# Kernel tuning notes

Hardware: AMD Instinct MI355X
Metric: run time of the kernel (lower is better)

## Reference

```python
import jax, jax.numpy as jnp
import numpy as np

# ---- module hyperparameters ----
B, L, F = 128, 720, 128
SEG = 24            # segment_length
NSEG = L // SEG     # 30 input segments
WIN = 15            # window_size
NPRED = 96 // SEG   # 4 prediction segments
D = 128             # encode_dim
H = 512             # hidden_dim
DECAY = 0.9
C = 1.0             # curvature
EPS = 1e-6
MAXN = 1.0 - 1e-5   # max radius of Poincare ball (c=1)
SQC = 1.0           # sqrt(C)

# ---- Poincare-ball manifold ops ----
def _sqnorm(x):
    return jnp.sum(x * x, axis=-1, keepdims=True)

def _norm(x):
    return jnp.sqrt(jnp.maximum(_sqnorm(x), EPS * EPS))

def _project(x):
    n = _norm(x)
    return jnp.where(n > MAXN, x * (MAXN / n), x)

def _artanh(x):
    return jnp.arctanh(jnp.clip(x, -1.0 + 1e-7, 1.0 - 1e-7))

def mobius_add(x, y):
    xy = jnp.sum(x * y, axis=-1, keepdims=True)
    x2, y2 = _sqnorm(x), _sqnorm(y)
    num = (1.0 + 2.0 * C * xy + C * y2) * x + (1.0 - C * x2) * y
    den = 1.0 + 2.0 * C * xy + C * C * x2 * y2
    return num / jnp.maximum(den, EPS)

def expmap0(v):
    n = _norm(v)
    return _project(jnp.tanh(SQC * n) * v / (SQC * n))

def logmap0(y):
    n = _norm(y)
    return _artanh(SQC * n) * y / (SQC * n)

def expmap(x, v):
    lam = 2.0 / jnp.maximum(1.0 - C * _sqnorm(x), EPS)
    n = _norm(v)
    second = jnp.tanh(SQC * lam * n / 2.0) * v / (SQC * n)
    return _project(mobius_add(x, second))

def logmap(x, y):
    d = mobius_add(-x, y)
    n = _norm(d)
    lam = 2.0 / jnp.maximum(1.0 - C * _sqnorm(x), EPS)
    return (2.0 / (SQC * lam)) * _artanh(SQC * n) * d / n


def setup_inputs() -> dict:
    key = jax.random.key(0)
    ks = jax.random.split(key, 12)
    s = 0.05
    return {
        'trend':           0.5 * jax.random.normal(ks[0], (B, L, F), jnp.float32),
        'seasonal_coarse': 0.5 * jax.random.normal(ks[1], (B, L, F), jnp.float32),
        'seasonal_fine':   0.5 * jax.random.normal(ks[2], (B, L, F), jnp.float32),
        'residual':        0.5 * jax.random.normal(ks[3], (B, L, F), jnp.float32),
        'W_t': s * jax.random.normal(ks[4], (SEG, D), jnp.float32), 'b_t': jnp.zeros((D,), jnp.float32),
        'W_c': s * jax.random.normal(ks[5], (SEG, D), jnp.float32), 'b_c': jnp.zeros((D,), jnp.float32),
        'W_f': s * jax.random.normal(ks[6], (SEG, D), jnp.float32), 'b_f': jnp.zeros((D,), jnp.float32),
        'W_r': s * jax.random.normal(ks[7], (SEG, D), jnp.float32), 'b_r': jnp.zeros((D,), jnp.float32),
        'alpha': jnp.array([0.5], jnp.float32),
        'W1': s * jax.random.normal(ks[8], (D, H), jnp.float32), 'b1': jnp.zeros((H,), jnp.float32),
        'W2': s * jax.random.normal(ks[9], (H, SEG), jnp.float32), 'b2': jnp.zeros((SEG,), jnp.float32),
    }


def reference(trend, seasonal_coarse, seasonal_fine, residual,
              W_t, b_t, W_c, b_c, W_f, b_f, W_r, b_r,
              alpha, W1, b1, W2, b2):
    b, l, f = trend.shape

    def collapse(x):  # [B,L,F] -> [B*F, NSEG, SEG]
        return x.transpose(0, 2, 1).reshape(b * f, NSEG, SEG)

    t_s, c_s, f_s, r_s = map(collapse, (trend, seasonal_coarse, seasonal_fine, residual))

    # per-segment tangent encoding (channel-independent, shared params)
    tan = (jnp.einsum('bns,sd->bnd', t_s, W_t) + b_t
           + jnp.einsum('bns,sd->bnd', c_s, W_c) + b_c
           + jnp.einsum('bns,sd->bnd', f_s, W_f) + b_f
           + jnp.einsum('bns,sd->bnd', r_s, W_r) + b_r)
    z = expmap0(tan)                     # [BF, NSEG, D] on the ball
    z_cur = z[:, -WIN:, :]

    idx = jnp.arange(WIN - 1, dtype=jnp.float32)
    w = DECAY ** (WIN - 2 - idx)
    w = w / w.sum()

    preds, latents = [], []
    for _ in range(NPRED):
        z_last = z_cur[:, -1]
        vel = logmap(z_cur[:, :-1], z_cur[:, 1:])
        avg_v = jnp.sum(vel * w[None, :, None], axis=1)    # [BF, D]
        z_next = expmap(z_last, alpha * avg_v)             # dynamics step
        latents.append(z_next)
        # reconstruction head: logmap0 -> MLP -> segment
        t0 = logmap0(z_next)
        seg = jax.nn.relu(t0 @ W1 + b1) @ W2 + b2          # [BF, SEG]
        preds.append(seg)
        z_cur = jnp.concatenate([z_cur[:, 1:], z_next[:, None]], axis=1)

    p = jnp.stack(preds, axis=1).reshape(b * f, NPRED * SEG)
    predictions = p.reshape(b, f, NPRED * SEG).transpose(0, 2, 1)  # [B, pred_len, F]
    return predictions
```

## Files before the change

kernel.cpp:

```cpp
#include <hip/hip_runtime.h>
#include <hip/hip_bf16.h>

namespace {
constexpr int kL = 720, kF = 128;
constexpr int kWin = 15;
constexpr float kEps = 1e-6f;
constexpr float kMaxN = 1.0f - 1e-5f;
constexpr int kT0off = 360;
constexpr int ZTR = 132;
constexpr int AROW = 104;
constexpr size_t kOffT0   = 0;
constexpr size_t kOffW1   = 16777216;
constexpr size_t kOffW2   = kOffW1 + 131072;
constexpr size_t kOffBt   = kOffW2 + 32768;
constexpr size_t kOffBsum = kOffBt + 73728;
constexpr size_t kOffHid  = 17825792;
constexpr size_t kWsSplit = kOffHid + 67108864;
}

typedef float f32x4 __attribute__((ext_vector_type(4)));
typedef short s16x8 __attribute__((ext_vector_type(8)));

__device__ __forceinline__ float rcp_f(float x) { return __builtin_amdgcn_rcpf(x); }
__device__ __forceinline__ float sqrt_f(float x) { return __builtin_amdgcn_sqrtf(x); }
__device__ __forceinline__ float tanh_f(float x) {
  float t = __builtin_amdgcn_exp2f(x * -2.8853900817779268f);
  return (1.0f - t) * rcp_f(1.0f + t);
}
__device__ __forceinline__ float artanh_f(float n) {
  float nc = fminf(n, 1.0f - 1e-7f);
  return 0.34657359027997264f * __builtin_amdgcn_logf((1.0f + nc) * rcp_f(1.0f - nc));
}

extern "C" __global__ __launch_bounds__(256)
void mwhf_prep(const float* __restrict__ W1, const float* __restrict__ W2,
               const float* __restrict__ W_t, const float* __restrict__ W_c,
               const float* __restrict__ W_f, const float* __restrict__ W_r,
               const float* __restrict__ b_t, const float* __restrict__ b_c,
               const float* __restrict__ b_f, const float* __restrict__ b_r,
               __hip_bfloat16* __restrict__ W1bf, __hip_bfloat16* __restrict__ W2bf,
               __hip_bfloat16* __restrict__ BtH, __hip_bfloat16* __restrict__ BtM,
               __hip_bfloat16* __restrict__ BtL, float* __restrict__ bsum)
{
  const int b = blockIdx.x, tid = threadIdx.x;
  if (b < 64) {
    const int n0 = b * 8;
    for (int e = tid; e < 1024; e += 256) {
      int n_l = e & 7, k = e >> 3;
      W1bf[(size_t)(n0 + n_l) * 128 + k] = __float2bfloat16(W1[(size_t)k * 512 + n0 + n_l]);
    }
  } else if (b < 68) {
    const int k0 = (b - 64) * 128;
    for (int e = tid; e < 4096; e += 256) {
      int p = e >> 7, k_l = e & 127;
      float v = (p < 24) ? W2[(size_t)(k0 + k_l) * 24 + p] : 0.0f;
      W2bf[(size_t)p * 512 + k0 + k_l] = __float2bfloat16(v);
    }
  } else if (b < 72) {
    const int st = b - 68;
    const float* src = (st == 0) ? W_t : (st == 1) ? W_c : (st == 2) ? W_f : W_r;
    for (int e = tid; e < 3072; e += 256) {
      int s = e >> 7, d = e & 127;
      float x = src[e];
      __hip_bfloat16 h = __float2bfloat16(x);
      float r1 = x - __bfloat162float(h);
      __hip_bfloat16 m = __float2bfloat16(r1);
      float r2 = r1 - __bfloat162float(m);
      const int o = d * 96 + st * 24 + s;
      BtH[o] = h;
      BtM[o] = m;
      BtL[o] = __float2bfloat16(r2);
    }
  } else {
    if (tid < 128) bsum[tid] = b_t[tid] + b_c[tid] + b_f[tid] + b_r[tid];
  }
}

extern "C" __global__ __launch_bounds__(256, 3)
void mwhf_k1(const float* __restrict__ trend,
             const float* __restrict__ seas_c,
             const float* __restrict__ seas_f,
             const float* __restrict__ resid,
             const __hip_bfloat16* __restrict__ BtH,
             const __hip_bfloat16* __restrict__ BtM,
             const __hip_bfloat16* __restrict__ BtL,
             const float* __restrict__ bsum,
             const float* __restrict__ alpha,
             __hip_bfloat16* __restrict__ t0_out)
{
  __shared__ __align__(16) char smem_raw[3 * 64 * AROW * 2];
  __shared__ float z2t[64];

  float* ublk = (float*)smem_raw;
  __hip_bfloat16* Ah = (__hip_bfloat16*)smem_raw;
  __hip_bfloat16* Am = Ah + 64 * AROW;
  __hip_bfloat16* Al = Am + 64 * AROW;

  const int tid = threadIdx.x;
  const int bix = blockIdx.x;
  const int bb = (bix & 7) * 16 + (bix >> 8);
  const int f0 = ((bix >> 3) & 31) * 4;
  const int row0 = bb * 128 + f0;

  for (int e = tid; e < 192; e += 256) {
    int rr = e / 48, cc = e - rr * 48;
    int off = (rr * 16 + 15) * AROW;
    ((unsigned int*)(Ah + off))[cc] = 0u;
    ((unsigned int*)(Am + off))[cc] = 0u;
    ((unsigned int*)(Al + off))[cc] = 0u;
  }
  {
    const float* ptrs[4] = {trend, seas_c, seas_f, resid};
    for (int e = tid; e < 1440; e += 256) {
      int seg = e / 96;
      int k = e - seg * 96;
      int st = k / 24, s = k - st * 24;
      const float* p = ptrs[st];
      float4 v = *(const float4*)&p[(size_t)(bb * kL + kT0off + seg * 24 + s) * kF + f0];
      float xv[4] = {v.x, v.y, v.z, v.w};
#pragma unroll
      for (int f = 0; f < 4; ++f) {
        int m = f * 16 + seg;
        __hip_bfloat16 h = __float2bfloat16(xv[f]);
        float r1 = xv[f] - __bfloat162float(h);
        __hip_bfloat16 mm = __float2bfloat16(r1);
        float r2 = r1 - __bfloat162float(mm);
        Ah[m * AROW + k] = h;
        Am[m * AROW + k] = mm;
        Al[m * AROW + k] = __float2bfloat16(r2);
      }
    }
  }
  __syncthreads();

  const int w = tid >> 6;
  const int lane = tid & 63;
  const int l16 = lane & 15, quad = lane >> 4;

  f32x4 acc0[8];
  float scale4[4], zz4[4];
  {
    f32x4 acc1[8];
    s16x8 ah[3], am[3], al[3];
    const int abase = (w * 16 + l16) * AROW + quad * 8;
#pragma unroll
    for (int ks = 0; ks < 3; ++ks) {
      ah[ks] = *(const s16x8*)(Ah + abase + ks * 32);
      am[ks] = *(const s16x8*)(Am + abase + ks * 32);
      al[ks] = *(const s16x8*)(Al + abase + ks * 32);
    }
#pragma unroll
    for (int t = 0; t < 8; ++t) { acc0[t] = (f32x4)0.f; acc1[t] = (f32x4)0.f; }
    const __hip_bfloat16* bhp = BtH + l16 * 96 + quad * 8;
    const __hip_bfloat16* bmp = BtM + l16 * 96 + quad * 8;
    const __hip_bfloat16* blp = BtL + l16 * 96 + quad * 8;
#pragma unroll
    for (int t = 0; t < 8; ++t) {
#pragma unroll
      for (int ks = 0; ks < 3; ++ks) {
        s16x8 bh = *(const s16x8*)(bhp + t * 1536 + ks * 32);
        s16x8 bm = *(const s16x8*)(bmp + t * 1536 + ks * 32);
        s16x8 bl = *(const s16x8*)(blp + t * 1536 + ks * 32);
        acc0[t] = __builtin_amdgcn_mfma_f32_16x16x32_bf16(ah[ks], bh, acc0[t], 0, 0, 0);
        acc1[t] = __builtin_amdgcn_mfma_f32_16x16x32_bf16(am[ks], bh, acc1[t], 0, 0, 0);
        acc1[t] = __builtin_amdgcn_mfma_f32_16x16x32_bf16(ah[ks], bm, acc1[t], 0, 0, 0);
        acc1[t] = __builtin_amdgcn_mfma_f32_16x16x32_bf16(al[ks], bh, acc1[t], 0, 0, 0);
        acc1[t] = __builtin_amdgcn_mfma_f32_16x16x32_bf16(ah[ks], bl, acc1[t], 0, 0, 0);
        acc1[t] = __builtin_amdgcn_mfma_f32_16x16x32_bf16(am[ks], bm, acc1[t], 0, 0, 0);
      }
    }
    float part[4] = {0.f, 0.f, 0.f, 0.f};
#pragma unroll
    for (int t = 0; t < 8; ++t) {
      float bv = bsum[t * 16 + l16];
#pragma unroll
      for (int r = 0; r < 4; ++r) {
        float v = (acc0[t][r] + acc1[t][r]) + bv;
        acc0[t][r] = v;
        part[r] += v * v;
      }
    }
#pragma unroll
    for (int m = 1; m <= 8; m <<= 1)
#pragma unroll
      for (int r = 0; r < 4; ++r) part[r] += __shfl_xor(part[r], m);
#pragma unroll
    for (int r = 0; r < 4; ++r) {
      float v2 = part[r];
      float nv = sqrt_f(fmaxf(v2, 1e-12f));
      float sc = tanh_f(nv) * rcp_f(nv);
      float y2 = sc * sc * v2;
      float yn = sqrt_f(fmaxf(y2, 1e-12f));
      float proj = (yn > kMaxN) ? (kMaxN * rcp_f(yn)) : 1.0f;
      scale4[r] = sc * proj;
      zz4[r] = y2 * proj * proj;
    }
  }
  __syncthreads();
  {
#pragma unroll
    for (int r = 0; r < 4; ++r) {
      int row = quad * 4 + r;
      if (row < kWin) {
#pragma unroll
        for (int t = 0; t < 8; ++t)
          ublk[(w * kWin + row) * ZTR + t * 16 + l16] = acc0[t][r] * scale4[r];
        if (l16 == 0) z2t[w * 16 + row] = zz4[r];
      }
    }
  }
  __syncthreads();

  {
    const int l = tid & 63;
    float zx[19], zy[19], z2a[19], pd[18];
#pragma unroll
    for (int j = 0; j < 15; ++j) {
      float2 v = *(const float2*)&ublk[(w * kWin + j) * ZTR + 2 * l];
      zx[j] = v.x; zy[j] = v.y;
      z2a[j] = z2t[w * 16 + j];
    }
#pragma unroll
    for (int j = 0; j < 14; ++j) pd[j] = zx[j] * zx[j + 1] + zy[j] * zy[j + 1];
#pragma unroll
    for (int m = 1; m <= 32; m <<= 1)
#pragma unroll
      for (int j = 0; j < 14; ++j) pd[j] += __shfl_xor(pd[j], m);

    const float alp = alpha[0];
    float W14[14];
    {
      float wv = 1.f, ss = 0.f;
      W14[13] = 1.f;
#pragma unroll
      for (int i = 12; i >= 0; --i) { wv *= 0.9f; W14[i] = wv; }
#pragma unroll
      for (int i = 0; i < 14; ++i) ss += W14[i];
      float inv = 1.f / ss;
#pragma unroll
      for (int i = 0; i < 14; ++i) W14[i] *= inv;
    }

#pragma unroll
    for (int it = 0; it < 4; ++it) {
      float avx = 0.f, avy = 0.f;
#pragma unroll
      for (int i = 0; i < 14; ++i) {
        const int j = it + i, y = j + 1;
        float x2 = z2a[j], y2 = z2a[y], dp = pd[j];
        float A = 1.f - 2.f * dp + y2;
        float Bq = 1.f - x2;
        float den = fmaxf(1.f - 2.f * dp + x2 * y2, kEps);
        float invd = rcp_f(den);
        float d2 = (A * A * x2 - 2.f * A * Bq * dp + Bq * Bq * y2) * (invd * invd);
        float n = sqrt_f(fmaxf(d2, 1e-12f));
        float coef = fmaxf(Bq, kEps) * artanh_f(n) * rcp_f(n);
        float wi = W14[i] * coef * invd;
        avx += wi * (Bq * zx[y] - A * zx[j]);
        avy += wi * (Bq * zy[y] - A * zy[j]);
      }
      float vx = alp * avx, vy = alp * avy;
      const int pl = it + 14;
      float x2l = z2a[pl];
      float v2 = vx * vx + vy * vy;
      float xdv = zx[pl] * vx + zy[pl] * vy;
#pragma unroll
      for (int m = 1; m <= 32; m <<= 1) {
        v2 += __shfl_xor(v2, m);
        xdv += __shfl_xor(xdv, m);
      }
      float nv = sqrt_f(fmaxf(v2, 1e-12f));
      float lam = 2.f * rcp_f(fmaxf(1.f - x2l, kEps));
      float co = tanh_f(0.5f * lam * nv) * rcp_f(nv);
      float s2 = co * co * v2;
      float xy = co * xdv;
      float P = 1.f + 2.f * xy + s2;
      float Q = 1.f - x2l;
      float den2 = fmaxf(1.f + 2.f * xy + x2l * s2, kEps);
      float invd2 = rcp_f(den2);
      float znx = (P * zx[pl] + Q * co * vx) * invd2;
      float zny = (P * zy[pl] + Q * co * vy) * invd2;
      float zn2 = (P * P * x2l + 2.f * P * Q * xy + Q * Q * s2) * (invd2 * invd2);
      float pdn = (P * x2l + Q * xy) * invd2;
      float yn = sqrt_f(fmaxf(zn2, 1e-12f));
      float proj = (yn > kMaxN) ? (kMaxN * rcp_f(yn)) : 1.f;
      znx *= proj; zny *= proj;
      zn2 *= proj * proj;
      pdn *= proj;
      zx[15 + it] = znx; zy[15 + it] = zny;
      z2a[15 + it] = zn2;
      pd[14 + it] = pdn;
      float n0 = sqrt_f(fmaxf(zn2, 1e-12f));
      float fac = artanh_f(n0) * rcp_f(n0);
      __hip_bfloat162 hv;
      hv.x = __float2bfloat16(fac * znx);
      hv.y = __float2bfloat16(fac * zny);
      *(__hip_bfloat162*)(t0_out + ((size_t)(row0 + w) * 4 + it) * 128 + 2 * l) = hv;
    }
  }
}

extern "C" __global__ __launch_bounds__(256, 4)
void mwhf_k2a(const __hip_bfloat16* __restrict__ t0g,
              const __hip_bfloat16* __restrict__ W1bf,
              const float* __restrict__ b1,
              __hip_bfloat16* __restrict__ hid)
{
  const int tid = threadIdx.x;
  const int w = tid >> 6, lane = tid & 63;
  const int l16 = lane & 15, quad = lane >> 4;
  const int mbase = blockIdx.x * 32;
  const int ng = w * 128;

  s16x8 afr[2][4];
#pragma unroll
  for (int s = 0; s < 2; ++s)
#pragma unroll
    for (int kc = 0; kc < 4; ++kc)
      afr[s][kc] = *(const s16x8*)(t0g + (size_t)(mbase + s * 16 + l16) * 128 + kc * 32 + quad * 8);

  f32x4 acc[2][8];
#pragma unroll
  for (int s = 0; s < 2; ++s)
#pragma unroll
    for (int t = 0; t < 8; ++t) acc[s][t] = (f32x4)0.f;

#pragma unroll
  for (int t = 0; t < 8; ++t) {
    const __hip_bfloat16* bp = W1bf + (size_t)(ng + t * 16 + l16) * 128 + quad * 8;
#pragma unroll
    for (int kc = 0; kc < 4; ++kc) {
      s16x8 bfr = *(const s16x8*)(bp + kc * 32);
      acc[0][t] = __builtin_amdgcn_mfma_f32_16x16x32_bf16(afr[0][kc], bfr, acc[0][t], 0, 0, 0);
      acc[1][t] = __builtin_amdgcn_mfma_f32_16x16x32_bf16(afr[1][kc], bfr, acc[1][t], 0, 0, 0);
    }
  }
#pragma unroll
  for (int t = 0; t < 8; ++t) {
    const int n = ng + t * 16 + l16;
    float bv = b1[n];
#pragma unroll
    for (int s = 0; s < 2; ++s)
#pragma unroll
      for (int r = 0; r < 4; ++r) {
        int m = mbase + s * 16 + quad * 4 + r;
        float h = fmaxf(acc[s][t][r] + bv, 0.f);
        hid[(size_t)m * 512 + n] = __float2bfloat16(h);
      }
  }
}

extern "C" __global__ __launch_bounds__(256, 4)
void mwhf_k2b(const __hip_bfloat16* __restrict__ hid,
              const __hip_bfloat16* __restrict__ W2bf,
              const float* __restrict__ b2,
              float* __restrict__ outp)
{
  const int tid = threadIdx.x;
  const int w = tid >> 6, lane = tid & 63;
  const int l16 = lane & 15, quad = lane >> 4;
  const int mb = (blockIdx.x * 4 + w) * 32;

  f32x4 acc[2][2];
#pragma unroll
  for (int s = 0; s < 2; ++s)
#pragma unroll
    for (int t = 0; t < 2; ++t) acc[s][t] = (f32x4)0.f;

#pragma unroll 4
  for (int kc = 0; kc < 16; ++kc) {
    s16x8 a0 = *(const s16x8*)(hid + (size_t)(mb + l16) * 512 + kc * 32 + quad * 8);
    s16x8 a1 = *(const s16x8*)(hid + (size_t)(mb + 16 + l16) * 512 + kc * 32 + quad * 8);
#pragma unroll
    for (int t = 0; t < 2; ++t) {
      s16x8 bfr = *(const s16x8*)(W2bf + (size_t)(t * 16 + l16) * 512 + kc * 32 + quad * 8);
      acc[0][t] = __builtin_amdgcn_mfma_f32_16x16x32_bf16(a0, bfr, acc[0][t], 0, 0, 0);
      acc[1][t] = __builtin_amdgcn_mfma_f32_16x16x32_bf16(a1, bfr, acc[1][t], 0, 0, 0);
    }
  }
#pragma unroll
  for (int t = 0; t < 2; ++t) {
    const int p = t * 16 + l16;
    if (p < 24) {
      float bv = b2[p];
#pragma unroll
      for (int s = 0; s < 2; ++s)
#pragma unroll
        for (int r = 0; r < 4; ++r) {
          int m = mb + s * 16 + quad * 4 + r;
          int bbi = m >> 9, it = m & 3, f = (m >> 2) & 127;
          outp[(size_t)bbi * 12288 + (it * 24 + p) * 128 + f] = acc[s][t][r] + bv;
        }
    }
  }
}

extern "C" __global__ __launch_bounds__(256)
void mwhf_k2f(const __hip_bfloat16* __restrict__ t0g,
              const __hip_bfloat16* __restrict__ W1bf,
              const __hip_bfloat16* __restrict__ W2bf,
              const float* __restrict__ b1, const float* __restrict__ b2,
              float* __restrict__ outp)
{
  __shared__ __align__(16) char smem[147456];
  s16x8* Av   = (s16x8*)smem;
  s16x8* W1v  = (s16x8*)(smem + 16384);
  s16x8* W2v  = (s16x8*)(smem + 16384);
  float* red  = (float*)(smem + 49152);
  __hip_bfloat16* hid = (__hip_bfloat16*)(smem + 81920);
  s16x8* hidv = (s16x8*)(smem + 81920);

  const int tid = threadIdx.x;
  const int m0 = blockIdx.x * 64;
  const int w = tid >> 6, lane = tid & 63;
  const int l16 = lane & 15, quad = lane >> 4;

  {
    const s16x8* src = (const s16x8*)(t0g + (size_t)m0 * 128);
    for (int e = tid; e < 1024; e += 256) {
      int m = e >> 4, c = e & 15;
      Av[m * 16 + (c ^ (m & 7))] = src[e];
    }
  }
  f32x4 acc[4][4];
  for (int nh = 0; nh < 2; ++nh) {
    __syncthreads();
    {
      const s16x8* src = (const s16x8*)W1bf + (size_t)nh * 4096;
      for (int e = tid; e < 4096; e += 256) {
        int n = e >> 4, c = e & 15;
        W1v[n * 16 + (c ^ (n & 7))] = src[e];
      }
    }
    __syncthreads();
#pragma unroll
    for (int s = 0; s < 4; ++s)
#pragma unroll
      for (int t = 0; t < 4; ++t) acc[s][t] = (f32x4)0.f;
#pragma unroll
    for (int ks = 0; ks < 4; ++ks) {
      s16x8 a[4];
#pragma unroll
      for (int s = 0; s < 4; ++s)
        a[s] = Av[(s * 16 + l16) * 16 + ((ks * 4 + quad) ^ (l16 & 7))];
#pragma unroll
      for (int t = 0; t < 4; ++t) {
        int nl = w * 64 + t * 16 + l16;
        s16x8 bfr = W1v[nl * 16 + ((ks * 4 + quad) ^ (nl & 7))];
#pragma unroll
        for (int s = 0; s < 4; ++s)
          acc[s][t] = __builtin_amdgcn_mfma_f32_16x16x32_bf16(a[s], bfr, acc[s][t], 0, 0, 0);
      }
    }
#pragma unroll
    for (int t = 0; t < 4; ++t) {
      int nabs = nh * 256 + w * 64 + t * 16 + l16;
      float bv = b1[nabs];
#pragma unroll
      for (int s = 0; s < 4; ++s)
#pragma unroll
        for (int r = 0; r < 4; ++r) {
          int m = s * 16 + quad * 4 + r;
          float h = fmaxf(acc[s][t][r] + bv, 0.f);
          hid[m * 512 + (nabs ^ ((m & 7) << 3))] = __float2bfloat16(h);
        }
    }
  }
  __syncthreads();
  {
    const s16x8* src = (const s16x8*)W2bf;
    for (int e = tid; e < 2048; e += 256) {
      int p = e >> 6, c = e & 63;
      W2v[p * 64 + (c ^ (p & 7))] = src[e];
    }
  }
  __syncthreads();
  {
    f32x4 a2[2];
    a2[0] = (f32x4)0.f; a2[1] = (f32x4)0.f;
    const int m = w * 16 + l16;
#pragma unroll 4
    for (int ks = 0; ks < 16; ++ks) {
      s16x8 av = hidv[m * 64 + ((ks * 4 + quad) ^ (l16 & 7))];
#pragma unroll
      for (int t = 0; t < 2; ++t) {
        s16x8 bfr = W2v[(t * 16 + l16) * 64 + ((ks * 4 + quad) ^ (l16 & 7))];
        a2[t] = __builtin_amdgcn_mfma_f32_16x16x32_bf16(av, bfr, a2[t], 0, 0, 0);
      }
    }
#pragma unroll
    for (int t = 0; t < 2; ++t)
#pragma unroll
      for (int r = 0; r < 4; ++r) {
        int p = t * 16 + l16;
        if (p < 24) red[(w * 16 + quad * 4 + r) * 25 + p] = a2[t][r];
      }
  }
  __syncthreads();
  {
    const int bbi = m0 >> 9;
    const int f0 = (m0 >> 2) & 127;
    for (int e = tid; e < 1536; e += 256) {
      int fi = e & 15;
      int rest = e >> 4;
      int p = rest % 24;
      int it = rest / 24;
      outp[(size_t)bbi * 12288 + rest * 128 + f0 + fi] = red[(fi * 4 + it) * 25 + p] + b2[p];
    }
  }
}

extern "C" void kernel_launch(void* const* d_in, const int* in_sizes, int n_in,
                              void* d_out, int out_size, void* d_ws, size_t ws_size,
                              hipStream_t stream) {
  (void)in_sizes; (void)n_in; (void)out_size;
  const float* trend = (const float*)d_in[0];
  const float* sc    = (const float*)d_in[1];
  const float* sf    = (const float*)d_in[2];
  const float* rs    = (const float*)d_in[3];
  const float* W_t   = (const float*)d_in[4];
  const float* b_t   = (const float*)d_in[5];
  const float* W_c   = (const float*)d_in[6];
  const float* b_c   = (const float*)d_in[7];
  const float* W_f   = (const float*)d_in[8];
  const float* b_f   = (const float*)d_in[9];
  const float* W_r   = (const float*)d_in[10];
  const float* b_r   = (const float*)d_in[11];
  const float* alpha = (const float*)d_in[12];
  const float* W1    = (const float*)d_in[13];
  const float* b1    = (const float*)d_in[14];
  const float* W2    = (const float*)d_in[15];
  const float* b2    = (const float*)d_in[16];

  char* ws = (char*)d_ws;
  __hip_bfloat16* t0   = (__hip_bfloat16*)(ws + kOffT0);
  __hip_bfloat16* W1bf = (__hip_bfloat16*)(ws + kOffW1);
  __hip_bfloat16* W2bf = (__hip_bfloat16*)(ws + kOffW2);
  __hip_bfloat16* BtH  = (__hip_bfloat16*)(ws + kOffBt);
  __hip_bfloat16* BtM  = BtH + 12288;
  __hip_bfloat16* BtL  = BtM + 12288;
  float* bsum = (float*)(ws + kOffBsum);
  __hip_bfloat16* hid = (__hip_bfloat16*)(ws + kOffHid);
  float* outp = (float*)d_out;

  hipLaunchKernelGGL(mwhf_prep, dim3(73), dim3(256), 0, stream,
                     W1, W2, W_t, W_c, W_f, W_r, b_t, b_c, b_f, b_r,
                     W1bf, W2bf, BtH, BtM, BtL, bsum);
  hipLaunchKernelGGL(mwhf_k1, dim3(4096), dim3(256), 0, stream,
                     trend, sc, sf, rs, BtH, BtM, BtL, bsum, alpha, t0);
  if (ws_size >= kWsSplit) {
    hipLaunchKernelGGL(mwhf_k2a, dim3(2048), dim3(256), 0, stream, t0, W1bf, b1, hid);
    hipLaunchKernelGGL(mwhf_k2b, dim3(512), dim3(256), 0, stream, hid, W2bf, b2, outp);
  } else {
    hipLaunchKernelGGL(mwhf_k2f, dim3(1024), dim3(256), 0, stream,
                       t0, W1bf, W2bf, b1, b2, outp);
  }
}
```

Baseline: 402.3 us.

## Spread velocity coefficients across lanes and use DPP reductions in k1

In the k1 dynamics loop, each lane now computes one of the 14 Möbius velocity coefficients instead of every lane computing all 14. The results are broadcast with readlane, and z2 and dot-product scalars move to shared memory. Cross-lane sums use DPP row ops plus two shuffles instead of xor-shuffle butterflies. The split-bf16 MFMA accumulators are merged into one, and launch bounds go up to 4 blocks per CU to cut register pressure and raise occupancy. The risks are slightly different fp32 summation order, and relying on in-wave LDS ordering when lane 0 writes values that other lanes read without a barrier.

```diff
diff --git a/kernel.cpp b/kernel.cpp
--- a/kernel.cpp
+++ b/kernel.cpp
@@ -30,6 +30,28 @@
 __device__ __forceinline__ float artanh_f(float n) {
   float nc = fminf(n, 1.0f - 1e-7f);
   return 0.34657359027997264f * __builtin_amdgcn_logf((1.0f + nc) * rcp_f(1.0f - nc));
+}
+
+template<int CTRL>
+__device__ __forceinline__ float dpp_add(float v) {
+  int mv = __builtin_amdgcn_update_dpp(0, __float_as_int(v), CTRL, 0xF, 0xF, false);
+  return v + __int_as_float(mv);
+}
+__device__ __forceinline__ float sum16(float v) {
+  v = dpp_add<0xB1>(v);
+  v = dpp_add<0x4E>(v);
+  v = dpp_add<0x141>(v);
+  v = dpp_add<0x128>(v);
+  return v;
+}
+__device__ __forceinline__ float sum64(float v) {
+  v = sum16(v);
+  v += __shfl_xor(v, 16);
+  v += __shfl_xor(v, 32);
+  return v;
+}
+__device__ __forceinline__ float rlane(float v, int i) {
+  return __int_as_float(__builtin_amdgcn_readlane(__float_as_int(v), i));
 }
 
 extern "C" __global__ __launch_bounds__(256)
@@ -76,7 +98,7 @@
   }
 }
 
-extern "C" __global__ __launch_bounds__(256, 3)
+extern "C" __global__ __launch_bounds__(256, 4)
 void mwhf_k1(const float* __restrict__ trend,
              const float* __restrict__ seas_c,
              const float* __restrict__ seas_f,
@@ -89,7 +111,8 @@
              __hip_bfloat16* __restrict__ t0_out)
 {
   __shared__ __align__(16) char smem_raw[3 * 64 * AROW * 2];
-  __shared__ float z2t[64];
+  __shared__ float z2s[80];
+  __shared__ float pds[80];
 
   float* ublk = (float*)smem_raw;
   __hip_bfloat16* Ah = (__hip_bfloat16*)smem_raw;
@@ -140,7 +163,6 @@
   f32x4 acc0[8];
   float scale4[4], zz4[4];
   {
-    f32x4 acc1[8];
     s16x8 ah[3], am[3], al[3];
     const int abase = (w * 16 + l16) * AROW + quad * 8;
 #pragma unroll
@@ -150,7 +172,7 @@
       al[ks] = *(const s16x8*)(Al + abase + ks * 32);
     }
 #pragma unroll
-    for (int t = 0; t < 8; ++t) { acc0[t] = (f32x4)0.f; acc1[t] = (f32x4)0.f; }
+    for (int t = 0; t < 8; ++t) acc0[t] = (f32x4)0.f;
     const __hip_bfloat16* bhp = BtH + l16 * 96 + quad * 8;
     const __hip_bfloat16* bmp = BtM + l16 * 96 + quad * 8;
     const __hip_bfloat16* blp = BtL + l16 * 96 + quad * 8;
@@ -162,11 +184,11 @@
         s16x8 bm = *(const s16x8*)(bmp + t * 1536 + ks * 32);
         s16x8 bl = *(const s16x8*)(blp + t * 1536 + ks * 32);
         acc0[t] = __builtin_amdgcn_mfma_f32_16x16x32_bf16(ah[ks], bh, acc0[t], 0, 0, 0);
-        acc1[t] = __builtin_amdgcn_mfma_f32_16x16x32_bf16(am[ks], bh, acc1[t], 0, 0, 0);
-        acc1[t] = __builtin_amdgcn_mfma_f32_16x16x32_bf16(ah[ks], bm, acc1[t], 0, 0, 0);
-        acc1[t] = __builtin_amdgcn_mfma_f32_16x16x32_bf16(al[ks], bh, acc1[t], 0, 0, 0);
-        acc1[t] = __builtin_amdgcn_mfma_f32_16x16x32_bf16(ah[ks], bl, acc1[t], 0, 0, 0);
-        acc1[t] = __builtin_amdgcn_mfma_f32_16x16x32_bf16(am[ks], bm, acc1[t], 0, 0, 0);
+        acc0[t] = __builtin_amdgcn_mfma_f32_16x16x32_bf16(am[ks], bh, acc0[t], 0, 0, 0);
+        acc0[t] = __builtin_amdgcn_mfma_f32_16x16x32_bf16(ah[ks], bm, acc0[t], 0, 0, 0);
+        acc0[t] = __builtin_amdgcn_mfma_f32_16x16x32_bf16(al[ks], bh, acc0[t], 0, 0, 0);
+        acc0[t] = __builtin_amdgcn_mfma_f32_16x16x32_bf16(ah[ks], bl, acc0[t], 0, 0, 0);
+        acc0[t] = __builtin_amdgcn_mfma_f32_16x16x32_bf16(am[ks], bm, acc0[t], 0, 0, 0);
       }
     }
     float part[4] = {0.f, 0.f, 0.f, 0.f};
@@ -175,15 +197,13 @@
       float bv = bsum[t * 16 + l16];
 #pragma unroll
       for (int r = 0; r < 4; ++r) {
-        float v = (acc0[t][r] + acc1[t][r]) + bv;
+        float v = acc0[t][r] + bv;
         acc0[t][r] = v;
         part[r] += v * v;
       }
     }
 #pragma unroll
-    for (int m = 1; m <= 8; m <<= 1)
-#pragma unroll
-      for (int r = 0; r < 4; ++r) part[r] += __shfl_xor(part[r], m);
+    for (int r = 0; r < 4; ++r) part[r] = sum16(part[r]);
 #pragma unroll
     for (int r = 0; r < 4; ++r) {
       float v2 = part[r];
@@ -205,70 +225,69 @@
 #pragma unroll
         for (int t = 0; t < 8; ++t)
           ublk[(w * kWin + row) * ZTR + t * 16 + l16] = acc0[t][r] * scale4[r];
-        if (l16 == 0) z2t[w * 16 + row] = zz4[r];
+        if (l16 == 0) z2s[w * 20 + row] = zz4[r];
       }
     }
   }
   __syncthreads();
 
   {
-    const int l = tid & 63;
-    float zx[19], zy[19], z2a[19], pd[18];
+    const int l = lane;
+    float zx[19], zy[19];
 #pragma unroll
     for (int j = 0; j < 15; ++j) {
       float2 v = *(const float2*)&ublk[(w * kWin + j) * ZTR + 2 * l];
       zx[j] = v.x; zy[j] = v.y;
-      z2a[j] = z2t[w * 16 + j];
-    }
-#pragma unroll
-    for (int j = 0; j < 14; ++j) pd[j] = zx[j] * zx[j + 1] + zy[j] * zy[j + 1];
-#pragma unroll
-    for (int m = 1; m <= 32; m <<= 1)
-#pragma unroll
-      for (int j = 0; j < 14; ++j) pd[j] += __shfl_xor(pd[j], m);
+    }
+    {
+      float pd[14];
+#pragma unroll
+      for (int j = 0; j < 14; ++j) pd[j] = zx[j] * zx[j + 1] + zy[j] * zy[j + 1];
+#pragma unroll
+      for (int j = 0; j < 14; ++j) pd[j] = sum64(pd[j]);
+      if (l == 0) {
+#pragma unroll
+        for (int j = 0; j < 14; ++j) pds[w * 20 + j] = pd[j];
+      }
+    }
 
     const float alp = alpha[0];
-    float W14[14];
-    {
-      float wv = 1.f, ss = 0.f;
-      W14[13] = 1.f;
-#pragma unroll
-      for (int i = 12; i >= 0; --i) { wv *= 0.9f; W14[i] = wv; }
-#pragma unroll
-      for (int i = 0; i < 14; ++i) ss += W14[i];
-      float inv = 1.f / ss;
-#pragma unroll
-      for (int i = 0; i < 14; ++i) W14[i] *= inv;
-    }
+    const float cw14 = (l < 14)
+        ? __builtin_amdgcn_exp2f((float)(13 - l) * -0.15200309344504997f) * 0.12966260f
+        : 0.f;
 
 #pragma unroll
     for (int it = 0; it < 4; ++it) {
-      float avx = 0.f, avy = 0.f;
-#pragma unroll
-      for (int i = 0; i < 14; ++i) {
-        const int j = it + i, y = j + 1;
-        float x2 = z2a[j], y2 = z2a[y], dp = pd[j];
-        float A = 1.f - 2.f * dp + y2;
-        float Bq = 1.f - x2;
+      float cA = 0.f, cB = 0.f, cW = 0.f;
+      if (l < 14) {
+        float dp = pds[w * 20 + it + l];
+        float x2 = z2s[w * 20 + it + l];
+        float y2 = z2s[w * 20 + it + l + 1];
+        cA = 1.f - 2.f * dp + y2;
+        cB = 1.f - x2;
         float den = fmaxf(1.f - 2.f * dp + x2 * y2, kEps);
         float invd = rcp_f(den);
-        float d2 = (A * A * x2 - 2.f * A * Bq * dp + Bq * Bq * y2) * (invd * invd);
+        float d2 = (cA * cA * x2 - 2.f * cA * cB * dp + cB * cB * y2) * (invd * invd);
         float n = sqrt_f(fmaxf(d2, 1e-12f));
-        float coef = fmaxf(Bq, kEps) * artanh_f(n) * rcp_f(n);
-        float wi = W14[i] * coef * invd;
-        avx += wi * (Bq * zx[y] - A * zx[j]);
-        avy += wi * (Bq * zy[y] - A * zy[j]);
+        float coef = fmaxf(cB, kEps) * artanh_f(n) * rcp_f(n);
+        cW = cw14 * coef * invd;
+      }
+      float avx = 0.f, avy = 0.f;
+#pragma unroll
+      for (int i = 0; i < 14; ++i) {
+        float sA = rlane(cA, i), sB = rlane(cB, i), sW = rlane(cW, i);
+        float tx = sB * zx[it + i + 1] - sA * zx[it + i];
+        float ty = sB * zy[it + i + 1] - sA * zy[it + i];
+        avx += sW * tx;
+        avy += sW * ty;
       }
       float vx = alp * avx, vy = alp * avy;
       const int pl = it + 14;
-      float x2l = z2a[pl];
+      float x2l = z2s[w * 20 + pl];
       float v2 = vx * vx + vy * vy;
       float xdv = zx[pl] * vx + zy[pl] * vy;
-#pragma unroll
-      for (int m = 1; m <= 32; m <<= 1) {
-        v2 += __shfl_xor(v2, m);
-        xdv += __shfl_xor(xdv, m);
-      }
+      v2 = sum64(v2);
+      xdv = sum64(xdv);
       float nv = sqrt_f(fmaxf(v2, 1e-12f));
       float lam = 2.f * rcp_f(fmaxf(1.f - x2l, kEps));
       float co = tanh_f(0.5f * lam * nv) * rcp_f(nv);
@@ -288,8 +307,10 @@
       zn2 *= proj * proj;
       pdn *= proj;
       zx[15 + it] = znx; zy[15 + it] = zny;
-      z2a[15 + it] = zn2;
-      pd[14 + it] = pdn;
+      if (l == 0) {
+        z2s[w * 20 + 15 + it] = zn2;
+        pds[w * 20 + 14 + it] = pdn;
+      }
       float n0 = sqrt_f(fmaxf(zn2, 1e-12f));
       float fac = artanh_f(n0) * rcp_f(n0);
       __hip_bfloat162 hv;
```

Measured after the change: 387.3 us. 1.04x faster.
